# Optimization experiments

Hardware: AMD Instinct MI355X
Metric: run time of the kernel (lower is better)

The kernel has to match this reference:

```python
import jax, jax.numpy as jnp
import numpy as np

B, I, H = 16384, 1024, 1024

def setup_inputs() -> dict:
    key = jax.random.key(0)
    ks = jax.random.split(key, 6)
    s_i = 1.0 / np.sqrt(I)
    s_h = 1.0 / np.sqrt(H)
    return {
        "incoming": jax.random.normal(ks[0], (B, I), dtype=jnp.float32),
        "old_h": jax.random.normal(ks[1], (B, H), dtype=jnp.float32),
        "old_c": jax.random.normal(ks[2], (B, H), dtype=jnp.float32),
        # 4 gates stacked: order [i, f, g, o] matching the torch ModuleList indices 0..3
        "Wi": jax.random.uniform(ks[3], (4, H, I), minval=-s_i, maxval=s_i, dtype=jnp.float32),
        "bi": jax.random.uniform(ks[4], (4, H), minval=-s_i, maxval=s_i, dtype=jnp.float32),
        "Wh": jax.random.uniform(ks[5], (4, H, H), minval=-s_h, maxval=s_h, dtype=jnp.float32),
    }

def reference(incoming, old_h, old_c, Wi, bi, Wh):
    # two batched GEMMs producing all 4 gate pre-activations: [4, B, H]
    gates = (jnp.einsum('bi,ghi->gbh', incoming, Wi)
             + jnp.einsum('bh,gkh->gbk', old_h, Wh)
             + bi[:, None, :])
    i = jax.nn.sigmoid(gates[0])
    f = jax.nn.sigmoid(gates[1])
    g = jnp.tanh(gates[2])
    o = jax.nn.sigmoid(gates[3])
    new_c = f * old_c + i * g
    new_h = o * jnp.tanh(new_c)
    return (new_h, (new_h, new_c))
```

## Files before the change

### kernel.cpp

```cpp
#include <hip/hip_runtime.h>
#include <hip/hip_bf16.h>
#include <math.h>

#define B_SZ 16384
#define H_SZ 1024
#define K_SZ 2048
#define OUT_PLANE ((size_t)B_SZ * H_SZ)

#define BM 256
#define BNH 64
#define BK 64
#define NKT (K_SZ / BK)

typedef __bf16 bf16;
typedef __attribute__((ext_vector_type(8))) __bf16 bf16x8;
typedef __attribute__((ext_vector_type(4))) float floatx4;

__device__ __forceinline__ void gload_lds16(const bf16* g, bf16* l) {
    __builtin_amdgcn_global_load_lds(
        (const __attribute__((address_space(1))) void*)g,
        (__attribute__((address_space(3))) void*)l, 16, 0, 0);
}

__device__ __forceinline__ void bar() { asm volatile("s_barrier" ::: "memory"); }
#define WAIT_VM(n) asm volatile("s_waitcnt vmcnt(" #n ")" ::: "memory")

__device__ __forceinline__ float sigmoidf_fast(float x) {
    return 1.f / (1.f + __expf(-x));
}
__device__ __forceinline__ float tanhf_fast(float x) {
    return 2.f / (1.f + __expf(-2.f * x)) - 1.f;
}

__global__ void cvt_all(const float* __restrict__ inc, const float* __restrict__ oh,
                        const float* __restrict__ Wi, const float* __restrict__ Wh,
                        bf16* __restrict__ X, bf16* __restrict__ W) {
    const size_t nX = (size_t)B_SZ * K_SZ;
    size_t t  = (size_t)blockIdx.x * blockDim.x + threadIdx.x;
    size_t e0 = t * 8;
    const float* src;
    bf16* dst;
    if (e0 < nX) {
        size_t b = e0 >> 11;
        int    k = (int)(e0 & 2047);
        src = (k < 1024) ? (inc + b * 1024 + k) : (oh + b * 1024 + (k - 1024));
        dst = X + e0;
    } else {
        size_t e = e0 - nX;
        size_t n = e >> 11;
        int    k = (int)(e & 2047);
        src = (k < 1024) ? (Wi + n * 1024 + k) : (Wh + n * 1024 + (k - 1024));
        dst = W + e;
    }
    floatx4 f0 = *(const floatx4*)src;
    floatx4 f1 = *(const floatx4*)(src + 4);
    bf16x8 o;
    o[0]=(bf16)f0[0]; o[1]=(bf16)f0[1]; o[2]=(bf16)f0[2]; o[3]=(bf16)f0[3];
    o[4]=(bf16)f1[0]; o[5]=(bf16)f1[1]; o[6]=(bf16)f1[2]; o[7]=(bf16)f1[3];
    *(bf16x8*)dst = o;
}

__device__ __forceinline__ void stageA(const bf16* xg, bf16* dst, int h, int ktn, int wv) {
    gload_lds16(xg + (size_t)(h * 64) * K_SZ + ktn, dst + (h * 64 + wv * 8) * BK);
    gload_lds16(xg + (size_t)(128 + h * 64) * K_SZ + ktn, dst + (128 + h * 64 + wv * 8) * BK);
}
__device__ __forceinline__ void stageB(const bf16* wg, bf16* dst, int hb, int ktn, int wv) {
    gload_lds16(wg + (size_t)((2 * hb) * 1024) * K_SZ + ktn, dst + ((2 * hb) * 64 + wv * 8) * BK);
    gload_lds16(wg + (size_t)((2 * hb + 1) * 1024) * K_SZ + ktn, dst + ((2 * hb + 1) * 64 + wv * 8) * BK);
}

__global__ __launch_bounds__(512, 2) void lstm_gemm(
    const bf16* __restrict__ X, const bf16* __restrict__ W,
    const float* __restrict__ bi, const float* __restrict__ oldc,
    float* __restrict__ out) {
    __shared__ bf16 As[2][BM * BK];
    __shared__ bf16 Bs[2][BM * BK];

    const int tid  = threadIdx.x;
    const int lane = tid & 63;
    const int wv   = tid >> 6;
    const int wm   = wv >> 2;
    const int wn   = wv & 3;
    const int q    = lane >> 4;
    const int r16  = lane & 15;
    const int lrow = lane >> 3;
    const int gch  = (lane & 7) ^ lrow;

    const int id = blockIdx.y * 16 + blockIdx.x;
    const int sw = (id & 7) * 128 + (id >> 3);
    const int h0    = (sw & 15) * BNH;
    const int brow0 = (sw >> 4) * BM;

    const bf16* xg = X + (size_t)(brow0 + wv * 8 + lrow) * K_SZ + gch * 8;
    const bf16* wg = W + (size_t)(h0 + wv * 8 + lrow) * K_SZ + gch * 8;

    floatx4 acc[8][4];
    #pragma unroll
    for (int mg = 0; mg < 8; ++mg)
        #pragma unroll
        for (int g = 0; g < 4; ++g) {
            floatx4 z = {0.f, 0.f, 0.f, 0.f};
            acc[mg][g] = z;
        }

    bf16x8 Af[4][2];
    bf16x8 Bf[4][2];

#define LDA(mh) do { \
    _Pragma("unroll") for (int m = 0; m < 4; ++m) { \
        const int row = wm * 128 + (mh) * 64 + m * 16 + r16; \
        const bf16* base = rA + (size_t)row * BK; \
        _Pragma("unroll") for (int ks = 0; ks < 2; ++ks) \
            Af[m][ks] = *(const bf16x8*)(base + (((ks * 4 + q) ^ (row & 7)) * 8)); \
    } } while (0)

#define LDB(nh) do { \
    _Pragma("unroll") for (int gg = 0; gg < 2; ++gg) { \
        const int row = ((nh) * 2 + gg) * 64 + wn * 16 + r16; \
        const bf16* base = rB + (size_t)row * BK; \
        _Pragma("unroll") for (int ks = 0; ks < 2; ++ks) \
            Bf[(nh) * 2 + gg][ks] = *(const bf16x8*)(base + (((ks * 4 + q) ^ (row & 7)) * 8)); \
    } } while (0)

#define MMA(mh, nh) do { \
    __builtin_amdgcn_s_setprio(1); \
    _Pragma("unroll") for (int m = 0; m < 4; ++m) \
    _Pragma("unroll") for (int gg = 0; gg < 2; ++gg) \
    _Pragma("unroll") for (int ks = 0; ks < 2; ++ks) \
        acc[(mh) * 4 + m][(nh) * 2 + gg] = __builtin_amdgcn_mfma_f32_16x16x32_bf16( \
            Af[m][ks], Bf[(nh) * 2 + gg][ks], acc[(mh) * 4 + m][(nh) * 2 + gg], 0, 0, 0); \
    __builtin_amdgcn_s_setprio(0); \
} while (0)

    const bf16* rA = As[0];
    const bf16* rB = Bs[0];
    bf16* wAp = As[1];
    bf16* wBp = Bs[1];

    stageA(xg, As[0], 0, 0, wv);
    stageB(wg, Bs[0], 0, 0, wv);
    stageB(wg, Bs[0], 1, 0, wv);
    stageA(xg, As[0], 1, 0, wv);

    for (int t = 0; t < NKT - 1; ++t) {
        const int ktn = (t + 1) * BK;
        WAIT_VM(4); bar();
        LDA(0); LDB(0);
        stageA(xg, wAp, 0, ktn, wv);
        MMA(0, 0);
        bar();
        WAIT_VM(4); bar();
        LDB(1);
        stageB(wg, wBp, 0, ktn, wv);
        MMA(0, 1);
        bar();
        WAIT_VM(4); bar();
        LDA(1);
        stageB(wg, wBp, 1, ktn, wv);
        MMA(1, 1);
        bar();
        stageA(xg, wAp, 1, ktn, wv);
        MMA(1, 0);
        bar();
        const bf16* tA = rA; rA = wAp; wAp = (bf16*)tA;
        const bf16* tB = rB; rB = wBp; wBp = (bf16*)tB;
    }

    WAIT_VM(4); bar();
    LDA(0); LDB(0);
    MMA(0, 0);
    bar();
    WAIT_VM(2); bar();
    LDB(1);
    MMA(0, 1);
    bar();
    WAIT_VM(0); bar();
    LDA(1);
    MMA(1, 1);
    bar();
    MMA(1, 0);

#undef LDA
#undef LDB
#undef MMA

    float* outh  = out;
    float* outh2 = out + OUT_PLANE;
    float* outc  = out + 2 * OUT_PLANE;
    const int h = h0 + wn * 16 + r16;
    const float b_i = bi[h];
    const float b_f = bi[H_SZ + h];
    const float b_g = bi[2 * H_SZ + h];
    const float b_o = bi[3 * H_SZ + h];
    #pragma unroll
    for (int mg = 0; mg < 8; ++mg) {
        const int brow = brow0 + wm * 128 + mg * 16 + q * 4;
        #pragma unroll
        for (int rr = 0; rr < 4; ++rr) {
            const size_t idx = (size_t)(brow + rr) * H_SZ + h;
            float gi = acc[mg][0][rr] + b_i;
            float gf = acc[mg][1][rr] + b_f;
            float gv_ = acc[mg][2][rr] + b_g;
            float go = acc[mg][3][rr] + b_o;
            float iv = sigmoidf_fast(gi);
            float fv = sigmoidf_fast(gf);
            float gv = tanhf_fast(gv_);
            float ov = sigmoidf_fast(go);
            float c  = fv * oldc[idx] + iv * gv;
            float hv = ov * tanhf_fast(c);
            outh[idx]  = hv;
            outh2[idx] = hv;
            outc[idx]  = c;
        }
    }
}

__global__ void lstm_fallback(const float* __restrict__ X, const float* __restrict__ Ho,
                              const float* __restrict__ Co, const float* __restrict__ Wi,
                              const float* __restrict__ bi, const float* __restrict__ Wh,
                              float* __restrict__ out) {
    int b = blockIdx.x;
    __shared__ float xs[1024], hs[1024];
    for (int k = threadIdx.x; k < 1024; k += blockDim.x) {
        xs[k] = X[(size_t)b * 1024 + k];
        hs[k] = Ho[(size_t)b * 1024 + k];
    }
    __syncthreads();
    for (int h = threadIdx.x; h < 1024; h += blockDim.x) {
        float g[4];
        for (int gg = 0; gg < 4; ++gg) {
            const float* wi = Wi + ((size_t)gg * 1024 + h) * 1024;
            const float* wh = Wh + ((size_t)gg * 1024 + h) * 1024;
            float acc = bi[gg * 1024 + h];
            for (int k = 0; k < 1024; ++k) acc += xs[k] * wi[k] + hs[k] * wh[k];
            g[gg] = acc;
        }
        float iv = sigmoidf_fast(g[0]);
        float fv = sigmoidf_fast(g[1]);
        float gv = tanhf_fast(g[2]);
        float ov = sigmoidf_fast(g[3]);
        float c  = fv * Co[(size_t)b * 1024 + h] + iv * gv;
        float hv = ov * tanhf_fast(c);
        size_t idx = (size_t)b * 1024 + h;
        out[idx] = hv;
        out[OUT_PLANE + idx] = hv;
        out[2 * OUT_PLANE + idx] = c;
    }
}

extern "C" void kernel_launch(void* const* d_in, const int* in_sizes, int n_in,
                              void* d_out, int out_size, void* d_ws, size_t ws_size,
                              hipStream_t stream) {
    const float* incoming = (const float*)d_in[0];
    const float* old_h    = (const float*)d_in[1];
    const float* old_c    = (const float*)d_in[2];
    const float* Wi       = (const float*)d_in[3];
    const float* bi       = (const float*)d_in[4];
    const float* Wh       = (const float*)d_in[5];
    float* out = (float*)d_out;

    const size_t nX = (size_t)B_SZ * K_SZ;
    const size_t nW = (size_t)4 * H_SZ * K_SZ;
    if (ws_size < (nX + nW) * sizeof(bf16)) {
        lstm_fallback<<<B_SZ, 256, 0, stream>>>(incoming, old_h, old_c, Wi, bi, Wh, out);
        return;
    }
    bf16* X = (bf16*)d_ws;
    bf16* W = X + nX;

    const int cvt_blocks = (int)((nX + nW) / 8 / 256);
    cvt_all<<<cvt_blocks, 256, 0, stream>>>(incoming, old_h, Wi, Wh, X, W);

    dim3 grid(H_SZ / BNH, B_SZ / BM);
    lstm_gemm<<<grid, 512, 0, stream>>>(X, W, bi, old_c, out);
}
```

Measured before the change: 600.4 us.

## Deepen GEMM prefetch to two tiles ahead with reordered stage schedule

Restructures the K-loop pipeline so half-tile global-to-LDS loads are issued up to two K-tiles ahead. Freed LDS halves of the current buffer are refilled as soon as they are consumed. Adds sched_barrier and explicit lgkmcnt waits to pin where MMA, LDS reads and barriers fall. The loop now covers all tiles with no epilogue, wrapping the prefetch index so it fetches redundant tiles at the end. This trades extra barriers and redundant tail loads for more memory-latency hiding, and the looser vmcnt accounting risks ordering mistakes.

```diff
diff --git a/kernel.cpp b/kernel.cpp
--- a/kernel.cpp
+++ b/kernel.cpp
@@ -22,8 +22,10 @@
         (__attribute__((address_space(3))) void*)l, 16, 0, 0);
 }
 
-__device__ __forceinline__ void bar() { asm volatile("s_barrier" ::: "memory"); }
-#define WAIT_VM(n) asm volatile("s_waitcnt vmcnt(" #n ")" ::: "memory")
+#define SBAR()   __builtin_amdgcn_s_barrier()
+#define SCHED0() __builtin_amdgcn_sched_barrier(0)
+#define WAIT_VM(n)   asm volatile("s_waitcnt vmcnt(" #n ")" ::: "memory")
+#define WAIT_LGKM0() asm volatile("s_waitcnt lgkmcnt(0)" ::: "memory")
 
 __device__ __forceinline__ float sigmoidf_fast(float x) {
     return 1.f / (1.f + __expf(-x));
@@ -132,53 +134,55 @@
     __builtin_amdgcn_s_setprio(0); \
 } while (0)
 
-    const bf16* rA = As[0];
-    const bf16* rB = Bs[0];
-    bf16* wAp = As[1];
-    bf16* wBp = Bs[1];
-
     stageA(xg, As[0], 0, 0, wv);
     stageB(wg, Bs[0], 0, 0, wv);
     stageB(wg, Bs[0], 1, 0, wv);
     stageA(xg, As[0], 1, 0, wv);
-
-    for (int t = 0; t < NKT - 1; ++t) {
-        const int ktn = (t + 1) * BK;
-        WAIT_VM(4); bar();
+    stageA(xg, As[1], 0, BK, wv);
+    stageB(wg, Bs[1], 0, BK, wv);
+    stageB(wg, Bs[1], 1, BK, wv);
+    WAIT_VM(10);
+    SBAR();
+
+    for (int t = 0; t < NKT; ++t) {
+        const bf16* rA = As[t & 1];
+        const bf16* rB = Bs[t & 1];
+        bf16* nA = As[(t + 1) & 1];
+        bf16* cA = (bf16*)As[t & 1];
+        bf16* cB = (bf16*)Bs[t & 1];
+        const int kt1 = ((t + 1) & (NKT - 1)) * BK;
+        const int kt2 = ((t + 2) & (NKT - 1)) * BK;
+
         LDA(0); LDB(0);
-        stageA(xg, wAp, 0, ktn, wv);
+        stageA(xg, nA, 1, kt1, wv);
+        WAIT_VM(10);
+        SBAR(); SCHED0();
+        WAIT_LGKM0(); SCHED0();
         MMA(0, 0);
-        bar();
-        WAIT_VM(4); bar();
+        SBAR();
+
         LDB(1);
-        stageB(wg, wBp, 0, ktn, wv);
+        stageA(xg, cA, 0, kt2, wv);
+        WAIT_VM(10);
+        SBAR(); SCHED0();
+        WAIT_LGKM0(); SCHED0();
         MMA(0, 1);
-        bar();
-        WAIT_VM(4); bar();
+        SBAR();
+
         LDA(1);
-        stageB(wg, wBp, 1, ktn, wv);
+        stageB(wg, cB, 0, kt2, wv);
+        SBAR(); SCHED0();
+        WAIT_LGKM0(); SCHED0();
         MMA(1, 1);
-        bar();
-        stageA(xg, wAp, 1, ktn, wv);
+        SBAR();
+
+        stageB(wg, cB, 1, kt2, wv);
+        WAIT_VM(10);
+        SBAR(); SCHED0();
         MMA(1, 0);
-        bar();
-        const bf16* tA = rA; rA = wAp; wAp = (bf16*)tA;
-        const bf16* tB = rB; rB = wBp; wBp = (bf16*)tB;
-    }
-
-    WAIT_VM(4); bar();
-    LDA(0); LDB(0);
-    MMA(0, 0);
-    bar();
-    WAIT_VM(2); bar();
-    LDB(1);
-    MMA(0, 1);
-    bar();
-    WAIT_VM(0); bar();
-    LDA(1);
-    MMA(1, 1);
-    bar();
-    MMA(1, 0);
+        SBAR();
+    }
+    WAIT_VM(0);
 
 #undef LDA
 #undef LDB
```

Result: slower. 637.7 us (+6.2%).
